# Kernel optimization log

Measured on AMD Instinct MI355X. Metric: run time of the kernel, lower is better.

The kernel has to match this reference:

```python
import jax, jax.numpy as jnp
import numpy as np

HIDDEN = 2048
HEADS = 16
HEAD = HIDDEN // HEADS  # 128
MB = 16                 # TTT mini-batch size
LR = 1.0                # inner (test-time) learning rate
ROPE_BASE = 10000.0
LN_EPS = 1e-5


def setup_inputs() -> dict:
    key = jax.random.key(0)
    ks = jax.random.split(key, 7)
    B, S = 4, 2048
    scale = HIDDEN ** -0.5
    x = jax.random.normal(ks[0], (B, S, HIDDEN), jnp.float32)
    Wk = jax.random.normal(ks[1], (HIDDEN, HIDDEN), jnp.float32) * scale
    Wv = jax.random.normal(ks[2], (HIDDEN, HIDDEN), jnp.float32) * scale
    Wo = jax.random.normal(ks[3], (HIDDEN, HIDDEN), jnp.float32) * scale
    ln_g = jnp.ones((HIDDEN,), jnp.float32)
    ln_b = jnp.zeros((HIDDEN,), jnp.float32)
    # initial TTT hidden-state weights, per (batch, head)
    W0 = jax.random.normal(ks[4], (B, HEADS, HEAD, HEAD), jnp.float32) * 0.02
    return {"x": x, "Wk": Wk, "Wv": Wv, "Wo": Wo, "ln_g": ln_g, "ln_b": ln_b, "W0": W0}


def _rotate_half(u):
    u1, u2 = jnp.split(u, 2, axis=-1)
    return jnp.concatenate([-u2, u1], axis=-1)


def _rope(k, seq_len):
    # k: [B, H, S, D]
    inv_freq = 1.0 / (ROPE_BASE ** (jnp.arange(0, HEAD, 2, dtype=jnp.float32) / HEAD))
    t = jnp.arange(seq_len, dtype=jnp.float32)
    freqs = t[:, None] * inv_freq[None, :]          # [S, D/2]
    emb = jnp.concatenate([freqs, freqs], axis=-1)  # [S, D]
    cos, sin = jnp.cos(emb), jnp.sin(emb)
    return k * cos[None, None] + _rotate_half(k) * sin[None, None]


def reference(x, Wk, Wv, Wo, ln_g, ln_b, W0):
    B, S, _ = x.shape
    # projections (nn.Linear convention: y = x @ W.T), split into heads
    k = (x @ Wk.T).reshape(B, S, HEADS, HEAD).transpose(0, 2, 1, 3)  # [B,H,S,D]
    v = (x @ Wv.T).reshape(B, S, HEADS, HEAD).transpose(0, 2, 1, 3)
    k = _rope(k, S)

    nc = S // MB
    # [nc, B, H, MB, D]
    kc = k.reshape(B, HEADS, nc, MB, HEAD).transpose(2, 0, 1, 3, 4)
    vc = v.reshape(B, HEADS, nc, MB, HEAD).transpose(2, 0, 1, 3, 4)

    def step(W, kv):
        k_c, v_c = kv                                   # [B,H,MB,D]
        pred = jnp.einsum('bhmd,bhde->bhme', k_c, W)    # f(k; W) = k W
        err = pred - v_c
        # grad of mean-MSE over (MB*D) elements w.r.t. W: 2/(MB*D) * k^T err
        grad = (2.0 / (MB * HEAD)) * jnp.einsum('bhmd,bhme->bhde', k_c, err)
        W_new = W - LR * grad                           # inner SGD step
        out = jnp.einsum('bhmd,bhde->bhme', k_c, W_new) # output with updated weights
        return W_new, out

    W_final, outs = jax.lax.scan(step, W0, (kc, vc))    # outs: [nc,B,H,MB,D]
    o = outs.transpose(1, 2, 0, 3, 4).reshape(B, HEADS, S, HEAD)
    o = o.transpose(0, 2, 1, 3).reshape(B, S, HIDDEN)

    # LayerNorm + output projection + residual
    mu = o.mean(-1, keepdims=True)
    var = o.var(-1, keepdims=True)
    o = (o - mu) / jnp.sqrt(var + LN_EPS) * ln_g + ln_b
    return x + o @ Wo.T
```

## Files before the change

kernel.cpp:

```cpp
#include <hip/hip_runtime.h>
#include <cstdint>
#include <cstddef>

typedef __attribute__((ext_vector_type(4))) float    f32x4;
typedef __attribute__((ext_vector_type(8))) __bf16   bf16x8;
typedef __attribute__((ext_vector_type(4))) short    s16x4;
typedef __attribute__((ext_vector_type(4))) uint32_t u32x4;
typedef __attribute__((ext_vector_type(2))) uint32_t u32x2;

__device__ __forceinline__ float bf2f(uint16_t h) {
    uint32_t u = ((uint32_t)h) << 16;
    return __builtin_bit_cast(float, u);
}
__device__ __forceinline__ uint16_t f2bf(float f) {
    uint32_t u = __builtin_bit_cast(uint32_t, f);
    uint32_t r = (u + 0x7fffu + ((u >> 16) & 1u)) >> 16;
    return (uint16_t)r;
}
__device__ __forceinline__ uint16_t f2bf_fast(float f) {
    __bf16 h = (__bf16)f;
    return __builtin_bit_cast(uint16_t, h);
}

__device__ __forceinline__ f32x4 mfma32(bf16x8 a, bf16x8 b, f32x4 c) {
    return __builtin_amdgcn_mfma_f32_16x16x32_bf16(a, b, c, 0, 0, 0);
}
__device__ __forceinline__ f32x4 mfma16(s16x4 a, s16x4 b, f32x4 c) {
    return __builtin_amdgcn_mfma_f32_16x16x16bf16_1k(a, b, c, 0, 0, 0);
}

__device__ __forceinline__ void gload16(const void* g, void* l) {
    __builtin_amdgcn_global_load_lds(
        (const __attribute__((address_space(1))) uint32_t*)g,
        (__attribute__((address_space(3))) uint32_t*)l, 16, 0, 0);
}

__global__ __launch_bounds__(256) void cvt_bf16(
    const float* __restrict__ s, uint16_t* __restrict__ d, int n4)
{
    int i = blockIdx.x * 256 + threadIdx.x;
    const int stride = gridDim.x * 256;
    for (; i < n4; i += stride) {
        f32x4 v = ((const f32x4*)s)[i];
        u32x2 p;
        p[0] = (uint32_t)f2bf(v[0]) | ((uint32_t)f2bf(v[1]) << 16);
        p[1] = (uint32_t)f2bf(v[2]) | ((uint32_t)f2bf(v[3]) << 16);
        ((u32x2*)d)[i] = p;
    }
}

template <bool F32OUT>
__global__ __launch_bounds__(512, 2) void gemm256(
    const uint16_t* __restrict__ A, const uint16_t* __restrict__ B,
    void* __restrict__ Cv, const float* __restrict__ R,
    int M, int N, int K)
{
    __shared__ __align__(16) uint16_t lA[2][256 * 64];
    __shared__ __align__(16) uint16_t lB[2][256 * 64];

    const int tid = threadIdx.x;
    const int w = tid >> 6, ln = tid & 63;
    const int l15 = ln & 15, q = ln >> 4;
    const int wm = w >> 2, wn = w & 3;
    const int m0 = blockIdx.y * 256, n0 = blockIdx.x * 256;

    const int srow = w * 32 + (ln >> 3);
    const int scol = ((ln & 7) ^ (ln >> 3)) * 8;
    const uint16_t* gA = A + (size_t)(m0 + srow) * K + scol;
    const uint16_t* gB = B + (size_t)(n0 + srow) * K + scol;

    f32x4 acc[8][4];
    #pragma unroll
    for (int i = 0; i < 8; i++)
        for (int j = 0; j < 4; j++)
            acc[i][j] = (f32x4){0.f, 0.f, 0.f, 0.f};

    const int xs  = (l15 & 7) * 8;
    const int aro = (wm * 128 + l15) * 64;
    const int bro = (wn * 64 + l15) * 64;
    const int k0o = (q * 8) ^ xs;
    const int k1o = (32 + q * 8) ^ xs;

    auto stage = [&](int t) {
        const int s = t & 1;
        const int kt = t * 64;
        #pragma unroll
        for (int i = 0; i < 4; i++)
            gload16(gA + (size_t)(i * 8) * K + kt, lA[s] + (w * 32 + i * 8) * 64);
        #pragma unroll
        for (int i = 0; i < 4; i++)
            gload16(gB + (size_t)(i * 8) * K + kt, lB[s] + (w * 32 + i * 8) * 64);
    };

    const int ntk = K >> 6;
    stage(0);
    __syncthreads();

    for (int t = 0; t < ntk; ++t) {
        const int s = t & 1;
        if (t + 1 < ntk) stage(t + 1);

        const uint16_t* As = lA[s];
        const uint16_t* Bs = lB[s];

        bf16x8 a0[8], b0[4];
        #pragma unroll
        for (int mt = 0; mt < 8; mt++)
            a0[mt] = __builtin_bit_cast(bf16x8,
                *(const u32x4*)(As + aro + mt * 1024 + k0o));
        #pragma unroll
        for (int nt2 = 0; nt2 < 4; nt2++)
            b0[nt2] = __builtin_bit_cast(bf16x8,
                *(const u32x4*)(Bs + bro + nt2 * 1024 + k0o));
        #pragma unroll
        for (int mt = 0; mt < 8; mt++)
            #pragma unroll
            for (int nt2 = 0; nt2 < 4; nt2++)
                acc[mt][nt2] = mfma32(a0[mt], b0[nt2], acc[mt][nt2]);

        bf16x8 a1[8], b1[4];
        #pragma unroll
        for (int mt = 0; mt < 8; mt++)
            a1[mt] = __builtin_bit_cast(bf16x8,
                *(const u32x4*)(As + aro + mt * 1024 + k1o));
        #pragma unroll
        for (int nt2 = 0; nt2 < 4; nt2++)
            b1[nt2] = __builtin_bit_cast(bf16x8,
                *(const u32x4*)(Bs + bro + nt2 * 1024 + k1o));
        #pragma unroll
        for (int mt = 0; mt < 8; mt++)
            #pragma unroll
            for (int nt2 = 0; nt2 < 4; nt2++)
                acc[mt][nt2] = mfma32(a1[mt], b1[nt2], acc[mt][nt2]);

        __syncthreads();
    }

    #pragma unroll
    for (int mt = 0; mt < 8; mt++)
        #pragma unroll
        for (int nt2 = 0; nt2 < 4; nt2++)
            #pragma unroll
            for (int r = 0; r < 4; r++) {
                int row = m0 + wm * 128 + mt * 16 + q * 4 + r;
                int col = n0 + wn * 64 + nt2 * 16 + l15;
                size_t idx = (size_t)row * N + col;
                float v = acc[mt][nt2][r];
                if (F32OUT) {
                    ((float*)Cv)[idx] = v + R[idx];
                } else {
                    ((uint16_t*)Cv)[idx] = f2bf(v);
                }
            }
}

__global__ __launch_bounds__(64) void repack(
    const uint16_t* __restrict__ kb, const uint16_t* __restrict__ vb,
    uint16_t* __restrict__ kp, uint16_t* __restrict__ kt,
    uint16_t* __restrict__ vt)
{
    const int g = blockIdx.x;
    const int c = g & 127, h = (g >> 7) & 15, b = g >> 11;
    const int ln = threadIdx.x;
    const int m = ln >> 2, cb = (ln & 3) * 32;
    const size_t tok = (size_t)b * 2048 + c * 16 + m;
    const int s = c * 16 + m;
    const uint16_t* krow = kb + tok * 2048 + h * 128;
    const uint16_t* vrow = vb + tok * 2048 + h * 128;

    u32x4 kraw[4], praw[4], vraw[4];
    for (int i = 0; i < 4; i++) {
        kraw[i] = *(const u32x4*)(krow + cb + 8 * i);
        praw[i] = *(const u32x4*)(krow + (cb ^ 64) + 8 * i);
        vraw[i] = *(const u32x4*)(vrow + cb + 8 * i);
    }
    const uint16_t* ku = (const uint16_t*)kraw;
    const uint16_t* pu = (const uint16_t*)praw;
    const uint16_t* vu = (const uint16_t*)vraw;

    uint16_t ko[32];
    for (int j = 0; j < 32; j++) {
        int col = cb + j;
        int p = col & 63;
        float invf = exp2f((float)p * (-13.287712379549449f / 64.0f));
        float a = (float)s * invf;
        float sn, cs;
        __sincosf(a, &sn, &cs);
        float u1 = bf2f(ku[j]), u2 = bf2f(pu[j]);
        float o = (col < 64) ? (u1 * cs - u2 * sn) : (u1 * cs + u2 * sn);
        ko[j] = f2bf(o);
    }

    uint16_t* kpg = kp + (size_t)g * 2048;
    uint16_t* ktg = kt + (size_t)g * 2048;
    uint16_t* vtg = vt + (size_t)g * 2048;
    for (int i = 0; i < 4; i++) {
        u32x4 pk;
        uint32_t* pw = (uint32_t*)&pk;
        for (int w = 0; w < 4; w++)
            pw[w] = (uint32_t)ko[8 * i + 2 * w] | ((uint32_t)ko[8 * i + 2 * w + 1] << 16);
        *(u32x4*)(kpg + m * 128 + cb + 8 * i) = pk;
    }
    for (int j = 0; j < 32; j++) {
        ktg[(cb + j) * 16 + m] = ko[j];
        vtg[(cb + j) * 16 + m] = vu[j];
    }
}

__global__ __launch_bounds__(64, 1) void ttt_scan(
    const uint16_t* __restrict__ kp, const uint16_t* __restrict__ kt,
    const uint16_t* __restrict__ vt, const float* __restrict__ W0,
    uint16_t* __restrict__ O)
{
    __shared__ __align__(16) uint16_t wbp[16 * 136];

    const int bid = blockIdx.x;
    const int g  = bid & 63;
    const int e0 = (bid >> 6) * 16;
    const int h = g & 15, b = g >> 4;
    const int ln = threadIdx.x;
    const int l15 = ln & 15, q = ln >> 4;

    f32x4 W[8];
    {
        const float* w0p = W0 + (size_t)g * 128 * 128;
        #pragma unroll
        for (int mt = 0; mt < 8; mt++)
            for (int r = 0; r < 4; r++)
                W[mt][r] = w0p[(size_t)(16 * mt + 4 * q + r) * 128 + e0 + l15];
    }
    #pragma unroll
    for (int mt = 0; mt < 8; mt++) {
        uint32_t p0 = (uint32_t)f2bf_fast(W[mt][0]) | ((uint32_t)f2bf_fast(W[mt][1]) << 16);
        uint32_t p1 = (uint32_t)f2bf_fast(W[mt][2]) | ((uint32_t)f2bf_fast(W[mt][3]) << 16);
        u32x2 pp; pp[0] = p0; pp[1] = p1;
        *(u32x2*)(wbp + l15 * 136 + 16 * mt + 4 * q) = pp;
    }

    const uint16_t* kpw = kp + (size_t)g * 128 * 2048;
    const uint16_t* ktw = kt + (size_t)g * 128 * 2048;
    const uint16_t* vtw = vt + (size_t)g * 128 * 2048;
    uint16_t*     obase = O  + (size_t)b * 2048 * 2048 + h * 128 + e0;

    auto loadset = [&](int c, u32x4* afr, u32x2* ktr, u32x2* vvr) {
        const uint16_t* kc = kpw + (size_t)c * 2048;
        const uint16_t* tc = ktw + (size_t)c * 2048;
        const uint16_t* vc = vtw + (size_t)c * 2048;
        #pragma unroll
        for (int ks = 0; ks < 4; ks++)
            afr[ks] = *(const u32x4*)(kc + l15 * 128 + ks * 32 + q * 8);
        #pragma unroll
        for (int mt = 0; mt < 8; mt++)
            ktr[mt] = *(const u32x2*)(tc + (16 * mt + l15) * 16 + 4 * q);
        vvr[0] = *(const u32x2*)(vc + (e0 + l15) * 16 + 4 * q);
    };

    auto step = [&](int c, const u32x4* afr, const u32x2* ktr, const u32x2* vvr) {
        const int s0 = c * 16;

        f32x4 accA = (f32x4){0.f, 0.f, 0.f, 0.f};
        f32x4 accB = (f32x4){0.f, 0.f, 0.f, 0.f};
        f32x4 gacA = (f32x4){0.f, 0.f, 0.f, 0.f};
        f32x4 gacB = (f32x4){0.f, 0.f, 0.f, 0.f};
        #pragma unroll
        for (int ks = 0; ks < 4; ks++) {
            bf16x8 a = __builtin_bit_cast(bf16x8, afr[ks]);
            bf16x8 bb = __builtin_bit_cast(bf16x8,
                *(const u32x4*)(wbp + l15 * 136 + ks * 32 + q * 8));
            if (ks & 1) { accB = mfma32(a, bb, accB); gacB = mfma32(a, a, gacB); }
            else        { accA = mfma32(a, bb, accA); gacA = mfma32(a, a, gacA); }
        }
        f32x4 acc, gacc;
        #pragma unroll
        for (int r = 0; r < 4; r++) { acc[r] = accA[r] + accB[r]; gacc[r] = gacA[r] + gacB[r]; }

        s16x4 vv = __builtin_bit_cast(s16x4, vvr[0]);
        s16x4 es, gf;
        #pragma unroll
        for (int r = 0; r < 4; r++) {
            es[r] = (short)f2bf_fast((bf2f((uint16_t)vv[r]) - acc[r]) * (1.0f / 1024.0f));
            gf[r] = (short)f2bf_fast(gacc[r]);
        }

        f32x4 o = mfma16(gf, es, acc);

        #pragma unroll
        for (int mt = 0; mt < 8; mt++) {
            s16x4 kf = __builtin_bit_cast(s16x4, ktr[mt]);
            W[mt] = mfma16(kf, es, W[mt]);
        }

        #pragma unroll
        for (int r = 0; r < 4; r++)
            obase[(size_t)(s0 + 4 * q + r) * 2048 + l15] = f2bf_fast(o[r]);

        #pragma unroll
        for (int mt = 0; mt < 8; mt++) {
            uint32_t p0 = (uint32_t)f2bf_fast(W[mt][0]) | ((uint32_t)f2bf_fast(W[mt][1]) << 16);
            uint32_t p1 = (uint32_t)f2bf_fast(W[mt][2]) | ((uint32_t)f2bf_fast(W[mt][3]) << 16);
            u32x2 pp; pp[0] = p0; pp[1] = p1;
            *(u32x2*)(wbp + l15 * 136 + 16 * mt + 4 * q) = pp;
        }
    };

    u32x4 afA[4], afB[4];
    u32x2 ktA[8], ktB[8];
    u32x2 vvA[1], vvB[1];
    loadset(0, afA, ktA, vvA);
    loadset(1, afB, ktB, vvB);

    for (int c = 0; c < 128; c += 2) {
        step(c, afA, ktA, vvA);
        if (c < 126) loadset(c + 2, afA, ktA, vvA);
        step(c + 1, afB, ktB, vvB);
        if (c < 126) loadset(c + 3, afB, ktB, vvB);
    }
}

__global__ __launch_bounds__(256) void ln_kernel(
    const uint16_t* __restrict__ X, const float* __restrict__ Gm,
    const float* __restrict__ Bt, uint16_t* __restrict__ Y)
{
    const int row = blockIdx.x, t = threadIdx.x;
    const uint16_t* xr = X + (size_t)row * 2048 + t * 8;
    u32x4 raw = *(const u32x4*)xr;
    const uint16_t* pr = (const uint16_t*)&raw;
    float v[8];
    float s = 0.f, s2 = 0.f;
    for (int i = 0; i < 8; i++) {
        v[i] = bf2f(pr[i]);
        s += v[i];
        s2 += v[i] * v[i];
    }
    for (int off = 32; off; off >>= 1) {
        s  += __shfl_down(s, off, 64);
        s2 += __shfl_down(s2, off, 64);
    }
    __shared__ float red[8];
    if ((t & 63) == 0) { red[(t >> 6) * 2] = s; red[(t >> 6) * 2 + 1] = s2; }
    __syncthreads();
    float ts  = red[0] + red[2] + red[4] + red[6];
    float ts2 = red[1] + red[3] + red[5] + red[7];
    float mu  = ts * (1.0f / 2048.0f);
    float var = ts2 * (1.0f / 2048.0f) - mu * mu;
    float inv = rsqrtf(var + 1e-5f);
    uint16_t outv[8];
    for (int i = 0; i < 8; i++) {
        float y = (v[i] - mu) * inv * Gm[t * 8 + i] + Bt[t * 8 + i];
        outv[i] = f2bf(y);
    }
    u32x4 ov;
    __builtin_memcpy(&ov, outv, 16);
    *(u32x4*)(Y + (size_t)row * 2048 + t * 8) = ov;
}

extern "C" void kernel_launch(void* const* d_in, const int* in_sizes, int n_in,
                              void* d_out, int out_size, void* d_ws, size_t ws_size,
                              hipStream_t stream)
{
    const float* x  = (const float*)d_in[0];
    const float* Wk = (const float*)d_in[1];
    const float* Wv = (const float*)d_in[2];
    const float* Wo = (const float*)d_in[3];
    const float* lg = (const float*)d_in[4];
    const float* lb = (const float*)d_in[5];
    const float* W0 = (const float*)d_in[6];
    float* out = (float*)d_out;

    const size_t NTOK = 8192, HID = 2048;
    uint16_t* xb   = (uint16_t*)d_ws;
    uint16_t* wbuf = xb + NTOK * HID;
    uint16_t* kb   = wbuf + HID * HID;
    uint16_t* vb   = kb + NTOK * HID;
    uint16_t* kt   = vb + NTOK * HID;
    uint16_t* vt   = kt + NTOK * HID;
    uint16_t* kp   = xb;
    uint16_t* ob   = (uint16_t*)d_out;
    uint16_t* lnb  = kb;

    dim3 grid(8, 32), blk(512);
    const int nX4 = (int)(NTOK * HID / 4), nW4 = (int)(HID * HID / 4);

    cvt_bf16<<<4096, 256, 0, stream>>>(x, xb, nX4);
    cvt_bf16<<<4096, 256, 0, stream>>>(Wk, wbuf, nW4);
    gemm256<false><<<grid, blk, 0, stream>>>(xb, wbuf, kb, nullptr, 8192, 2048, 2048);
    cvt_bf16<<<4096, 256, 0, stream>>>(Wv, wbuf, nW4);
    gemm256<false><<<grid, blk, 0, stream>>>(xb, wbuf, vb, nullptr, 8192, 2048, 2048);
    repack<<<8192, 64, 0, stream>>>(kb, vb, kp, kt, vt);
    ttt_scan<<<512, 64, 0, stream>>>(kp, kt, vt, W0, ob);
    ln_kernel<<<8192, 256, 0, stream>>>(ob, lg, lb, lnb);
    cvt_bf16<<<4096, 256, 0, stream>>>(Wo, wbuf, nW4);
    gemm256<true><<<grid, blk, 0, stream>>>(lnb, wbuf, out, x, 8192, 2048, 2048);
}
```

Baseline: 538.6 us.

## Keep bf16 TTT weight fragments in registers instead of LDS round-trip

The scan kernel no longer writes the updated bf16 copy of W to shared memory each step and reads it back for the prediction matmul. The prediction now uses 16x16x16 MFMAs whose B operand layout matches the W accumulator layout, so the bf16 fragment converted from the accumulator is used directly. This removes LDS stores and loads from the serial per-chunk dependency chain, at the cost of twice as many smaller MFMAs for the prediction and Gram products, and a different K load pattern.

After: 541.2 us. No clear change (+0.5%).

```diff
diff --git a/kernel.cpp b/kernel.cpp
--- a/kernel.cpp
+++ b/kernel.cpp
@@ -212,8 +212,6 @@
     const uint16_t* __restrict__ vt, const float* __restrict__ W0,
     uint16_t* __restrict__ O)
 {
-    __shared__ __align__(16) uint16_t wbp[16 * 136];
-
     const int bid = blockIdx.x;
     const int g  = bid & 63;
     const int e0 = (bid >> 6) * 16;
@@ -222,6 +220,7 @@
     const int l15 = ln & 15, q = ln >> 4;
 
     f32x4 W[8];
+    s16x4 Wb[8];
     {
         const float* w0p = W0 + (size_t)g * 128 * 128;
         #pragma unroll
@@ -230,90 +229,80 @@
                 W[mt][r] = w0p[(size_t)(16 * mt + 4 * q + r) * 128 + e0 + l15];
     }
     #pragma unroll
-    for (int mt = 0; mt < 8; mt++) {
-        uint32_t p0 = (uint32_t)f2bf_fast(W[mt][0]) | ((uint32_t)f2bf_fast(W[mt][1]) << 16);
-        uint32_t p1 = (uint32_t)f2bf_fast(W[mt][2]) | ((uint32_t)f2bf_fast(W[mt][3]) << 16);
-        u32x2 pp; pp[0] = p0; pp[1] = p1;
-        *(u32x2*)(wbp + l15 * 136 + 16 * mt + 4 * q) = pp;
-    }
+    for (int mt = 0; mt < 8; mt++)
+        for (int r = 0; r < 4; r++)
+            Wb[mt][r] = (short)f2bf_fast(W[mt][r]);
 
     const uint16_t* kpw = kp + (size_t)g * 128 * 2048;
     const uint16_t* ktw = kt + (size_t)g * 128 * 2048;
     const uint16_t* vtw = vt + (size_t)g * 128 * 2048;
     uint16_t*     obase = O  + (size_t)b * 2048 * 2048 + h * 128 + e0;
 
-    auto loadset = [&](int c, u32x4* afr, u32x2* ktr, u32x2* vvr) {
+    auto loadset = [&](int c, u32x2* ka, u32x2* ktf, u32x2* vv) {
         const uint16_t* kc = kpw + (size_t)c * 2048;
         const uint16_t* tc = ktw + (size_t)c * 2048;
         const uint16_t* vc = vtw + (size_t)c * 2048;
         #pragma unroll
-        for (int ks = 0; ks < 4; ks++)
-            afr[ks] = *(const u32x4*)(kc + l15 * 128 + ks * 32 + q * 8);
-        #pragma unroll
-        for (int mt = 0; mt < 8; mt++)
-            ktr[mt] = *(const u32x2*)(tc + (16 * mt + l15) * 16 + 4 * q);
-        vvr[0] = *(const u32x2*)(vc + (e0 + l15) * 16 + 4 * q);
+        for (int dt = 0; dt < 8; dt++)
+            ka[dt] = *(const u32x2*)(kc + l15 * 128 + 16 * dt + 4 * q);
+        #pragma unroll
+        for (int mt = 0; mt < 8; mt++)
+            ktf[mt] = *(const u32x2*)(tc + (16 * mt + l15) * 16 + 4 * q);
+        vv[0] = *(const u32x2*)(vc + (e0 + l15) * 16 + 4 * q);
     };
 
-    auto step = [&](int c, const u32x4* afr, const u32x2* ktr, const u32x2* vvr) {
+    auto step = [&](int c, const u32x2* ka, const u32x2* ktf, const u32x2* vv) {
         const int s0 = c * 16;
 
-        f32x4 accA = (f32x4){0.f, 0.f, 0.f, 0.f};
-        f32x4 accB = (f32x4){0.f, 0.f, 0.f, 0.f};
-        f32x4 gacA = (f32x4){0.f, 0.f, 0.f, 0.f};
-        f32x4 gacB = (f32x4){0.f, 0.f, 0.f, 0.f};
-        #pragma unroll
-        for (int ks = 0; ks < 4; ks++) {
-            bf16x8 a = __builtin_bit_cast(bf16x8, afr[ks]);
-            bf16x8 bb = __builtin_bit_cast(bf16x8,
-                *(const u32x4*)(wbp + l15 * 136 + ks * 32 + q * 8));
-            if (ks & 1) { accB = mfma32(a, bb, accB); gacB = mfma32(a, a, gacB); }
-            else        { accA = mfma32(a, bb, accA); gacA = mfma32(a, a, gacA); }
+        f32x4 pA = (f32x4){0.f, 0.f, 0.f, 0.f};
+        f32x4 pB = (f32x4){0.f, 0.f, 0.f, 0.f};
+        f32x4 gA = (f32x4){0.f, 0.f, 0.f, 0.f};
+        f32x4 gB = (f32x4){0.f, 0.f, 0.f, 0.f};
+        #pragma unroll
+        for (int dt = 0; dt < 8; dt++) {
+            s16x4 kf = __builtin_bit_cast(s16x4, ka[dt]);
+            if (dt & 1) { pB = mfma16(kf, Wb[dt], pB); gB = mfma16(kf, kf, gB); }
+            else        { pA = mfma16(kf, Wb[dt], pA); gA = mfma16(kf, kf, gA); }
         }
-        f32x4 acc, gacc;
-        #pragma unroll
-        for (int r = 0; r < 4; r++) { acc[r] = accA[r] + accB[r]; gacc[r] = gacA[r] + gacB[r]; }
-
-        s16x4 vv = __builtin_bit_cast(s16x4, vvr[0]);
+        f32x4 p, gacc;
+        #pragma unroll
+        for (int r = 0; r < 4; r++) { p[r] = pA[r] + pB[r]; gacc[r] = gA[r] + gB[r]; }
+
+        s16x4 vvs = __builtin_bit_cast(s16x4, vv[0]);
         s16x4 es, gf;
         #pragma unroll
         for (int r = 0; r < 4; r++) {
-            es[r] = (short)f2bf_fast((bf2f((uint16_t)vv[r]) - acc[r]) * (1.0f / 1024.0f));
+            es[r] = (short)f2bf_fast((bf2f((uint16_t)vvs[r]) - p[r]) * (1.0f / 1024.0f));
             gf[r] = (short)f2bf_fast(gacc[r]);
         }
 
-        f32x4 o = mfma16(gf, es, acc);
+        f32x4 o = mfma16(gf, es, p);
 
         #pragma unroll
         for (int mt = 0; mt < 8; mt++) {
-            s16x4 kf = __builtin_bit_cast(s16x4, ktr[mt]);
+            s16x4 kf = __builtin_bit_cast(s16x4, ktf[mt]);
             W[mt] = mfma16(kf, es, W[mt]);
+            #pragma unroll
+            for (int r = 0; r < 4; r++)
+                Wb[mt][r] = (short)f2bf_fast(W[mt][r]);
         }
 
         #pragma unroll
         for (int r = 0; r < 4; r++)
             obase[(size_t)(s0 + 4 * q + r) * 2048 + l15] = f2bf_fast(o[r]);
-
-        #pragma unroll
-        for (int mt = 0; mt < 8; mt++) {
-            uint32_t p0 = (uint32_t)f2bf_fast(W[mt][0]) | ((uint32_t)f2bf_fast(W[mt][1]) << 16);
-            uint32_t p1 = (uint32_t)f2bf_fast(W[mt][2]) | ((uint32_t)f2bf_fast(W[mt][3]) << 16);
-            u32x2 pp; pp[0] = p0; pp[1] = p1;
-            *(u32x2*)(wbp + l15 * 136 + 16 * mt + 4 * q) = pp;
-        }
     };
 
-    u32x4 afA[4], afB[4];
+    u32x2 kaA[8], kaB[8];
     u32x2 ktA[8], ktB[8];
     u32x2 vvA[1], vvB[1];
-    loadset(0, afA, ktA, vvA);
-    loadset(1, afB, ktB, vvB);
+    loadset(0, kaA, ktA, vvA);
+    loadset(1, kaB, ktB, vvB);
 
     for (int c = 0; c < 128; c += 2) {
-        step(c, afA, ktA, vvA);
-        if (c < 126) loadset(c + 2, afA, ktA, vvA);
-        step(c + 1, afB, ktB, vvB);
-        if (c < 126) loadset(c + 3, afB, ktB, vvB);
+        step(c, kaA, ktA, vvA);
+        if (c < 126) loadset(c + 2, kaA, ktA, vvA);
+        step(c + 1, kaB, ktB, vvB);
+        if (c < 126) loadset(c + 3, kaB, ktB, vvB);
     }
 }
 
```
